# Kernel tuning notes

Measured on AMD Instinct MI355X. Metric: run time of the kernel, lower is better.

The kernel has to match this reference:

```python
import jax, jax.numpy as jnp
import numpy as np

NEG_INF = -9e15


def setup_inputs() -> dict:
    key = jax.random.key(0)
    k1, k2, k3, k4 = jax.random.split(key, 4)
    N, F_in, H, F_out = 4096, 512, 8, 64
    node_features = jax.random.normal(k1, (N, F_in), dtype=jnp.float32)
    adj_matrix = jax.random.randint(k2, (N, N), 0, 2, dtype=jnp.int32)
    # ensure self-loops so every row has at least one unmasked entry
    adj_matrix = jnp.maximum(adj_matrix, jnp.eye(N, dtype=jnp.int32))
    W = jax.random.normal(k3, (H, F_in, F_out), dtype=jnp.float32) * 0.05
    a = jax.random.normal(k4, (H, 2 * F_out), dtype=jnp.float32) * 0.05
    return {"node_features": node_features, "adj_matrix": adj_matrix, "W": W, "a": a}


def reference(node_features, adj_matrix, W, a):
    alpha = 0.2
    H, F_in, F_out = W.shape
    # Per-head linear projection: [H, N, F_out]
    Wh = jnp.einsum("nf,hfo->hno", node_features, W)
    # Attention logits e_ij = LeakyReLU(a1 . Wh_i + a2 . Wh_j)
    f_src = jnp.einsum("hno,ho->hn", Wh, a[:, :F_out])   # [H, N]
    f_dst = jnp.einsum("hno,ho->hn", Wh, a[:, F_out:])   # [H, N]
    e = jax.nn.leaky_relu(f_src[:, :, None] + f_dst[:, None, :], negative_slope=alpha)  # [H, N, N]
    # Mask by adjacency, softmax over neighbors
    masked = jnp.where(adj_matrix[None, :, :] > 0, e, NEG_INF)
    attn = jax.nn.softmax(masked, axis=-1)               # [H, N, N]
    # Aggregate neighbor features per head
    h_prime = jnp.einsum("hnm,hmo->hno", attn, Wh)       # [H, N, F_out]
    # Concat heads along feature dim -> [N, H*F_out]
    return jnp.transpose(h_prime, (1, 0, 2)).reshape(h_prime.shape[1], H * F_out)
```

## Files before the change

kernel.cpp:

```cpp
#include <hip/hip_runtime.h>
#include <stdint.h>


#define NN 4096
#define FIN 512
#define NH 8
#define FO 64

typedef _Float16 f16x8 __attribute__((ext_vector_type(8)));
typedef _Float16 f16x2 __attribute__((ext_vector_type(2)));
typedef __attribute__((ext_vector_type(4))) float f32x4;

union H8 { f16x8 v; f16x2 p[4]; unsigned u[4]; };
union U2 { unsigned u; f16x2 v; };

#define GLOAD_LDS16(g, l)                                                          \
  __builtin_amdgcn_global_load_lds((__attribute__((address_space(1))) const void*)(g), \
                                   (__attribute__((address_space(3))) void*)(l), 16, 0, 0)
#define GLOAD_LDS4(g, l)                                                           \
  __builtin_amdgcn_global_load_lds((__attribute__((address_space(1))) const void*)(g), \
                                   (__attribute__((address_space(3))) void*)(l), 4, 0, 0)

__device__ __forceinline__ unsigned short f2h(float f) {
  _Float16 h = (_Float16)f;
  return __builtin_bit_cast(unsigned short, h);
}

__global__ __launch_bounds__(256) void prep_kernel(
    const float* __restrict__ X, const int* __restrict__ adj, const float* __restrict__ W,
    const float* __restrict__ a,
    unsigned short* __restrict__ Xh, unsigned short* __restrict__ WbT,
    unsigned* __restrict__ adjbitsT, unsigned short* __restrict__ WAh) {
  int bid = blockIdx.x, tid = threadIdx.x;
  if (bid < 2048) {
    int item = bid * 256 + tid;
    int jt = item >> 12, r = item & 4095;
    const int* p = adj + (size_t)r * NN + jt * 32;
    unsigned bits = 0;
#pragma unroll
    for (int b = 0; b < 32; b += 4) {
      int4 v = *(const int4*)(p + b);
      bits |= (unsigned)(v.x & 1) << b;
      bits |= (unsigned)(v.y & 1) << (b + 1);
      bits |= (unsigned)(v.z & 1) << (b + 2);
      bits |= (unsigned)(v.w & 1) << (b + 3);
    }
    adjbitsT[item] = bits;
  } else if (bid < 4096) {
    int item = (bid - 2048) * 256 + tid;
    float4 v = ((const float4*)X)[item];
    ushort4 o;
    o.x = f2h(v.x); o.y = f2h(v.y); o.z = f2h(v.z); o.w = f2h(v.w);
    ((ushort4*)Xh)[item] = o;
  } else if (bid < 5120) {
    int item = (bid - 4096) * 256 + tid;
    int h = item >> 15, rem = item & 32767, o = rem >> 9, k = rem & 511;
    WbT[item] = f2h(W[h * (FIN * FO) + k * FO + o]);
  } else {
    int item = (bid - 5120) * 256 + tid;
    int h = item >> 10, which = (item >> 9) & 1, k = item & 511;
    const float4* wp = (const float4*)(W + ((size_t)h * FIN + k) * FO);
    const float4* ap = (const float4*)(a + h * 128 + which * 64);
    float s = 0.f;
#pragma unroll
    for (int o4 = 0; o4 < 16; ++o4) {
      float4 w4 = wp[o4], a4 = ap[o4];
      s += w4.x * a4.x + w4.y * a4.y + w4.z * a4.z + w4.w * a4.w;
    }
    WAh[(h * 2 + which) * FIN + k] = f2h(s);
  }
}

__global__ __launch_bounds__(256, 4) void proj_sd_kernel(
    const unsigned short* __restrict__ Xh, const unsigned short* __restrict__ WbT,
    const unsigned short* __restrict__ WAh,
    unsigned short* __restrict__ Whfrag, float2* __restrict__ ABf,
    unsigned short* __restrict__ E1h, unsigned short* __restrict__ E2h) {
  int lane = threadIdx.x & 63, wave = threadIdx.x >> 6;
  int row16 = lane & 15, grp = lane >> 4;
  if (blockIdx.y == 8) {
    int i0 = (blockIdx.x * 4 + wave) * 16;
    f32x4 acc = {0, 0, 0, 0};
    const unsigned short* xb = Xh + (size_t)(i0 + row16) * FIN + grp * 8;
    const unsigned short* wb = WAh + row16 * FIN + grp * 8;
#pragma unroll
    for (int k0 = 0; k0 < FIN; k0 += 32)
      acc = __builtin_amdgcn_mfma_f32_16x16x32_f16(*(const f16x8*)(xb + k0),
                                                   *(const f16x8*)(wb + k0), acc, 0, 0, 0);
    int hh = row16 >> 1;
#pragma unroll
    for (int reg = 0; reg < 4; ++reg) {
      int rr = i0 + grp * 4 + reg;
      float v = acc[reg];
      if (row16 & 1) {
        E1h[hh * NN + rr] = f2h(__expf(v));
        E2h[hh * NN + rr] = f2h(__expf(0.2f * v));
      } else {
        ABf[hh * NN + rr] = make_float2(__expf(v), __expf(0.2f * v));
      }
    }
    return;
  }
  int h = blockIdx.y;
  int i0 = blockIdx.x * 64 + wave * 16;
  f32x4 acc[4] = {{0,0,0,0},{0,0,0,0},{0,0,0,0},{0,0,0,0}};
  const unsigned short* xb = Xh + (size_t)(i0 + row16) * FIN + grp * 8;
  const unsigned short* wb = WbT + h * (FO * FIN) + row16 * FIN + grp * 8;
#pragma unroll 4
  for (int k0 = 0; k0 < FIN; k0 += 32) {
    f16x8 af = *(const f16x8*)(xb + k0);
#pragma unroll
    for (int cb = 0; cb < 4; ++cb)
      acc[cb] = __builtin_amdgcn_mfma_f32_16x16x32_f16(
          af, *(const f16x8*)(wb + cb * 16 * FIN + k0), acc[cb], 0, 0, 0);
  }
  int jt = i0 >> 5;
  int kk0 = (i0 & 31) + grp * 4;
  int tl = (kk0 >> 3) * 16 + row16;
  int e0 = kk0 & 7;
#pragma unroll
  for (int cb = 0; cb < 4; ++cb) {
    ushort4 pk;
    pk.x = f2h(acc[cb][0]); pk.y = f2h(acc[cb][1]);
    pk.z = f2h(acc[cb][2]); pk.w = f2h(acc[cb][3]);
    *(ushort4*)(Whfrag + (((size_t)h * 128 + jt) * 4 + cb) * 512 + tl * 8 + e0) = pk;
  }
}

#define SEGB 4608
#define E_OFF 4096
#define A_OFF 4224

__global__ __launch_bounds__(512, 8) void gat_kernel(
    const unsigned* __restrict__ adjbitsT, const unsigned short* __restrict__ Whfrag,
    const float2* __restrict__ ABf, const unsigned short* __restrict__ E1h,
    const unsigned short* __restrict__ E2h, float* __restrict__ out) {
  __shared__ __align__(16) char lds[8 * SEGB];
  int h = blockIdx.y;
  int lane = threadIdx.x & 63, wave = threadIdx.x >> 6;
  int row16 = lane & 15, grp = lane >> 4;
  int rt = wave >> 2, jseg = wave & 3;
  int r0 = blockIdx.x * 32;
  int i0 = r0 + rt * 16;
  int r = i0 + row16;
  float2 ab = ABf[h * NN + r];
  _Float16 Ah1 = (_Float16)(0.5f * ab.x);
  _Float16 Bh1 = (_Float16)(0.5f * ab.y);
  f16x2 Ah = {Ah1, Ah1}, Bh = {Bh1, Bh1};

  H8 ones;
#pragma unroll
  for (int k = 0; k < 4; ++k) ones.u[k] = 0x3C003C00u;

  const unsigned short* wsrc =
      Whfrag + (size_t)h * 262144 + (size_t)jseg * 32 * 2048 + lane * 8;
  const unsigned short* esrc =
      ((lane & 4) ? E2h : E1h) + h * NN + jseg * 1024 + (lane & 3) * 8;
  const unsigned* asrc = adjbitsT + (size_t)(jseg * 32) * NN + r0 + lane;

  f32x4 a0 = {0,0,0,0}, a1 = {0,0,0,0}, a2 = {0,0,0,0}, ad = {0,0,0,0}, aden = {0,0,0,0};

  char* seg0 = lds + (jseg * 2 + 0) * SEGB;
  char* seg1 = lds + (jseg * 2 + 1) * SEGB;

  auto stage = [&](char* seg, int p) {
    if (rt == 0) {
      const unsigned short* bs = wsrc + (size_t)p * 2048;
      GLOAD_LDS16(bs, seg);
      GLOAD_LDS16(bs + 512, seg + 1024);
      GLOAD_LDS16(bs + 1024, seg + 2048);
      GLOAD_LDS16(bs + 1536, seg + 3072);
    } else {
      if (lane < 32) GLOAD_LDS4(asrc + (size_t)p * NN, seg + A_OFF);
      if (lane < 8)  GLOAD_LDS16(esrc + p * 32, seg + E_OFF);
    }
  };

  auto compute = [&](const char* seg) {
    unsigned bw = *(const unsigned*)(seg + A_OFF + (rt * 16 + row16) * 4);
    unsigned bb = (bw >> (grp * 8)) & 0xffu;
    unsigned t32 = bb | (bb << 15);
    H8 e1, e2;
    e1.v = *(const f16x8*)(seg + E_OFF + grp * 16);
    e2.v = *(const f16x8*)(seg + E_OFF + 64 + grp * 16);
    const char* bp = seg + lane * 16;
    f16x8 b0 = *(const f16x8*)(bp);
    f16x8 b1 = *(const f16x8*)(bp + 1024);
    f16x8 b2 = *(const f16x8*)(bp + 2048);
    f16x8 b3 = *(const f16x8*)(bp + 3072);
    H8 af;
#pragma unroll
    for (int k = 0; k < 4; ++k) {
      U2 m;
      m.u = (t32 << (14 - 2 * k)) & 0x40004000u;
      af.p[k] = __builtin_elementwise_max(Ah * e1.p[k], Bh * e2.p[k]) * m.v;
    }
    a0   = __builtin_amdgcn_mfma_f32_16x16x32_f16(af.v, b0, a0, 0, 0, 0);
    a1   = __builtin_amdgcn_mfma_f32_16x16x32_f16(af.v, b1, a1, 0, 0, 0);
    a2   = __builtin_amdgcn_mfma_f32_16x16x32_f16(af.v, b2, a2, 0, 0, 0);
    aden = __builtin_amdgcn_mfma_f32_16x16x32_f16(af.v, ones.v, aden, 0, 0, 0);
    ad   = __builtin_amdgcn_mfma_f32_16x16x32_f16(af.v, b3, ad, 0, 0, 0);
  };

  stage(seg0, 0);
  __syncthreads();
#pragma unroll 1
  for (int p2 = 0; p2 < 16; ++p2) {
    stage(seg1, 2 * p2 + 1);
    compute(seg0);
    __syncthreads();
    if (p2 < 15) stage(seg0, 2 * p2 + 2);
    compute(seg1);
    __syncthreads();
  }

  float* red = (float*)lds;
  if (jseg != 0) {
    float* q = red + (((jseg - 1) * 2 + rt) * 64 + lane) * 20;
    *(f32x4*)(q +  0) = a0;
    *(f32x4*)(q +  4) = a1;
    *(f32x4*)(q +  8) = a2;
    *(f32x4*)(q + 12) = ad;
    *(f32x4*)(q + 16) = aden;
  }
  __syncthreads();
  if (jseg == 0) {
#pragma unroll
    for (int s = 0; s < 3; ++s) {
      const float* q = red + ((s * 2 + rt) * 64 + lane) * 20;
      a0   += *(const f32x4*)(q +  0);
      a1   += *(const f32x4*)(q +  4);
      a2   += *(const f32x4*)(q +  8);
      ad   += *(const f32x4*)(q + 12);
      aden += *(const f32x4*)(q + 16);
    }
#pragma unroll
    for (int reg = 0; reg < 4; ++reg) {
      float inv = 1.0f / aden[reg];
      int row = i0 + grp * 4 + reg;
      float* op = out + (size_t)row * (NH * FO) + h * FO + row16;
      op[0]  = a0[reg] * inv;
      op[16] = a1[reg] * inv;
      op[32] = a2[reg] * inv;
      op[48] = ad[reg] * inv;
    }
  }
}

extern "C" void kernel_launch(void* const* d_in, const int* in_sizes, int n_in,
                              void* d_out, int out_size, void* d_ws, size_t ws_size,
                              hipStream_t stream) {
  const float* X  = (const float*)d_in[0];
  const int* adj  = (const int*)d_in[1];
  const float* W  = (const float*)d_in[2];
  const float* a  = (const float*)d_in[3];
  float* out = (float*)d_out;
  char* ws = (char*)d_ws;

  unsigned short* Xh     = (unsigned short*)(ws + 0);
  unsigned short* WbT    = (unsigned short*)(ws + 4194304);
  unsigned* adjbitsT     = (unsigned*)(ws + 4718592);
  unsigned short* Whfrag = (unsigned short*)(ws + 6815744);
  unsigned short* WAh    = (unsigned short*)(ws + 11010048);
  float2* ABf            = (float2*)(ws + 11026432);
  unsigned short* E1h    = (unsigned short*)(ws + 11288576);
  unsigned short* E2h    = (unsigned short*)(ws + 11354112);

  prep_kernel<<<5152, 256, 0, stream>>>(X, adj, W, a, Xh, WbT, adjbitsT, WAh);
  proj_sd_kernel<<<dim3(64, 9), 256, 0, stream>>>(Xh, WbT, WAh, Whfrag, ABf, E1h, E2h);
  gat_kernel<<<dim3(128, 8), 512, 0, stream>>>(adjbitsT, Whfrag, ABf, E1h, E2h, out);
}
```

Measured before the change: 84.69 us.

## Split-K projection waves and process both row tiles per wave in GAT

The projection kernel now splits the K dimension across two wave groups, reduces the partial sums through LDS, and runs on a flat grid with 512-thread blocks. The attention kernel drops to 4 waves per block, and each wave computes both 16-row tiles. This reuses each loaded B fragment and attention coefficient across twice the rows and cuts LDS reads per MFMA. In exchange, register pressure rises from doubled accumulators and there are fewer waves for latency hiding.

```diff
diff --git a/kernel.cpp b/kernel.cpp
--- a/kernel.cpp
+++ b/kernel.cpp
@@ -71,15 +71,17 @@
   }
 }
 
-__global__ __launch_bounds__(256, 4) void proj_sd_kernel(
+__global__ __launch_bounds__(512, 4) void proj_sd_kernel(
     const unsigned short* __restrict__ Xh, const unsigned short* __restrict__ WbT,
     const unsigned short* __restrict__ WAh,
     unsigned short* __restrict__ Whfrag, float2* __restrict__ ABf,
     unsigned short* __restrict__ E1h, unsigned short* __restrict__ E2h) {
+  __shared__ float red[4 * 64 * 20];
   int lane = threadIdx.x & 63, wave = threadIdx.x >> 6;
   int row16 = lane & 15, grp = lane >> 4;
-  if (blockIdx.y == 8) {
-    int i0 = (blockIdx.x * 4 + wave) * 16;
+  int bx = blockIdx.x;
+  if (bx >= 512) {
+    int i0 = ((bx - 512) * 8 + wave) * 16;
     f32x4 acc = {0, 0, 0, 0};
     const unsigned short* xb = Xh + (size_t)(i0 + row16) * FIN + grp * 8;
     const unsigned short* wb = WAh + row16 * FIN + grp * 8;
@@ -101,29 +103,42 @@
     }
     return;
   }
-  int h = blockIdx.y;
-  int i0 = blockIdx.x * 64 + wave * 16;
+  int kh = wave >> 2, jb = wave & 3;
+  int job = bx * 4 + jb;
+  int h = job & 7, rt = job >> 3;
+  int i0 = rt * 16;
   f32x4 acc[4] = {{0,0,0,0},{0,0,0,0},{0,0,0,0},{0,0,0,0}};
-  const unsigned short* xb = Xh + (size_t)(i0 + row16) * FIN + grp * 8;
-  const unsigned short* wb = WbT + h * (FO * FIN) + row16 * FIN + grp * 8;
-#pragma unroll 4
-  for (int k0 = 0; k0 < FIN; k0 += 32) {
+  const unsigned short* xb = Xh + (size_t)(i0 + row16) * FIN + kh * 256 + grp * 8;
+  const unsigned short* wb = WbT + h * (FO * FIN) + row16 * FIN + kh * 256 + grp * 8;
+#pragma unroll
+  for (int k0 = 0; k0 < 256; k0 += 32) {
     f16x8 af = *(const f16x8*)(xb + k0);
 #pragma unroll
     for (int cb = 0; cb < 4; ++cb)
       acc[cb] = __builtin_amdgcn_mfma_f32_16x16x32_f16(
           af, *(const f16x8*)(wb + cb * 16 * FIN + k0), acc[cb], 0, 0, 0);
   }
-  int jt = i0 >> 5;
-  int kk0 = (i0 & 31) + grp * 4;
-  int tl = (kk0 >> 3) * 16 + row16;
-  int e0 = kk0 & 7;
-#pragma unroll
-  for (int cb = 0; cb < 4; ++cb) {
-    ushort4 pk;
-    pk.x = f2h(acc[cb][0]); pk.y = f2h(acc[cb][1]);
-    pk.z = f2h(acc[cb][2]); pk.w = f2h(acc[cb][3]);
-    *(ushort4*)(Whfrag + (((size_t)h * 128 + jt) * 4 + cb) * 512 + tl * 8 + e0) = pk;
+  if (kh == 1) {
+    float* q = red + (jb * 64 + lane) * 20;
+#pragma unroll
+    for (int cb = 0; cb < 4; ++cb) *(f32x4*)(q + cb * 4) = acc[cb];
+  }
+  __syncthreads();
+  if (kh == 0) {
+    const float* q = red + (jb * 64 + lane) * 20;
+#pragma unroll
+    for (int cb = 0; cb < 4; ++cb) acc[cb] += *(const f32x4*)(q + cb * 4);
+    int jt = i0 >> 5;
+    int kk0 = (i0 & 31) + grp * 4;
+    int tl = (kk0 >> 3) * 16 + row16;
+    int e0 = kk0 & 7;
+#pragma unroll
+    for (int cb = 0; cb < 4; ++cb) {
+      ushort4 pk;
+      pk.x = f2h(acc[cb][0]); pk.y = f2h(acc[cb][1]);
+      pk.z = f2h(acc[cb][2]); pk.w = f2h(acc[cb][3]);
+      *(ushort4*)(Whfrag + (((size_t)h * 128 + jt) * 4 + cb) * 512 + tl * 8 + e0) = pk;
+    }
   }
 }
 
@@ -131,22 +146,20 @@
 #define E_OFF 4096
 #define A_OFF 4224
 
-__global__ __launch_bounds__(512, 8) void gat_kernel(
+__global__ __launch_bounds__(256, 4) void gat_kernel(
     const unsigned* __restrict__ adjbitsT, const unsigned short* __restrict__ Whfrag,
     const float2* __restrict__ ABf, const unsigned short* __restrict__ E1h,
     const unsigned short* __restrict__ E2h, float* __restrict__ out) {
   __shared__ __align__(16) char lds[8 * SEGB];
   int h = blockIdx.y;
-  int lane = threadIdx.x & 63, wave = threadIdx.x >> 6;
+  int lane = threadIdx.x & 63, jseg = threadIdx.x >> 6;
   int row16 = lane & 15, grp = lane >> 4;
-  int rt = wave >> 2, jseg = wave & 3;
   int r0 = blockIdx.x * 32;
-  int i0 = r0 + rt * 16;
-  int r = i0 + row16;
-  float2 ab = ABf[h * NN + r];
-  _Float16 Ah1 = (_Float16)(0.5f * ab.x);
-  _Float16 Bh1 = (_Float16)(0.5f * ab.y);
-  f16x2 Ah = {Ah1, Ah1}, Bh = {Bh1, Bh1};
+  float2 abL = ABf[h * NN + r0 + row16];
+  float2 abH = ABf[h * NN + r0 + 16 + row16];
+  _Float16 aL = (_Float16)(0.5f * abL.x), bL = (_Float16)(0.5f * abL.y);
+  _Float16 aH = (_Float16)(0.5f * abH.x), bH = (_Float16)(0.5f * abH.y);
+  f16x2 AhL = {aL, aL}, BhL = {bL, bL}, AhH = {aH, aH}, BhH = {bH, bH};
 
   H8 ones;
 #pragma unroll
@@ -158,28 +171,29 @@
       ((lane & 4) ? E2h : E1h) + h * NN + jseg * 1024 + (lane & 3) * 8;
   const unsigned* asrc = adjbitsT + (size_t)(jseg * 32) * NN + r0 + lane;
 
-  f32x4 a0 = {0,0,0,0}, a1 = {0,0,0,0}, a2 = {0,0,0,0}, ad = {0,0,0,0}, aden = {0,0,0,0};
+  f32x4 l0 = {0,0,0,0}, l1 = {0,0,0,0}, l2 = {0,0,0,0}, ld = {0,0,0,0}, lden = {0,0,0,0};
+  f32x4 h0 = {0,0,0,0}, h1 = {0,0,0,0}, h2 = {0,0,0,0}, hd = {0,0,0,0}, hden = {0,0,0,0};
 
   char* seg0 = lds + (jseg * 2 + 0) * SEGB;
   char* seg1 = lds + (jseg * 2 + 1) * SEGB;
 
   auto stage = [&](char* seg, int p) {
-    if (rt == 0) {
-      const unsigned short* bs = wsrc + (size_t)p * 2048;
-      GLOAD_LDS16(bs, seg);
-      GLOAD_LDS16(bs + 512, seg + 1024);
-      GLOAD_LDS16(bs + 1024, seg + 2048);
-      GLOAD_LDS16(bs + 1536, seg + 3072);
-    } else {
-      if (lane < 32) GLOAD_LDS4(asrc + (size_t)p * NN, seg + A_OFF);
-      if (lane < 8)  GLOAD_LDS16(esrc + p * 32, seg + E_OFF);
-    }
+    const unsigned short* bs = wsrc + (size_t)p * 2048;
+    GLOAD_LDS16(bs, seg);
+    GLOAD_LDS16(bs + 512, seg + 1024);
+    GLOAD_LDS16(bs + 1024, seg + 2048);
+    GLOAD_LDS16(bs + 1536, seg + 3072);
+    if (lane < 32) GLOAD_LDS4(asrc + (size_t)p * NN, seg + A_OFF);
+    if (lane < 8)  GLOAD_LDS16(esrc + p * 32, seg + E_OFF);
   };
 
   auto compute = [&](const char* seg) {
-    unsigned bw = *(const unsigned*)(seg + A_OFF + (rt * 16 + row16) * 4);
-    unsigned bb = (bw >> (grp * 8)) & 0xffu;
-    unsigned t32 = bb | (bb << 15);
+    unsigned bwL = *(const unsigned*)(seg + A_OFF + row16 * 4);
+    unsigned bwH = *(const unsigned*)(seg + A_OFF + 64 + row16 * 4);
+    unsigned bbL = (bwL >> (grp * 8)) & 0xffu;
+    unsigned bbH = (bwH >> (grp * 8)) & 0xffu;
+    unsigned tL = bbL | (bbL << 15);
+    unsigned tH = bbH | (bbH << 15);
     H8 e1, e2;
     e1.v = *(const f16x8*)(seg + E_OFF + grp * 16);
     e2.v = *(const f16x8*)(seg + E_OFF + 64 + grp * 16);
@@ -188,18 +202,27 @@
     f16x8 b1 = *(const f16x8*)(bp + 1024);
     f16x8 b2 = *(const f16x8*)(bp + 2048);
     f16x8 b3 = *(const f16x8*)(bp + 3072);
-    H8 af;
+    H8 afL, afH;
 #pragma unroll
     for (int k = 0; k < 4; ++k) {
-      U2 m;
-      m.u = (t32 << (14 - 2 * k)) & 0x40004000u;
-      af.p[k] = __builtin_elementwise_max(Ah * e1.p[k], Bh * e2.p[k]) * m.v;
-    }
-    a0   = __builtin_amdgcn_mfma_f32_16x16x32_f16(af.v, b0, a0, 0, 0, 0);
-    a1   = __builtin_amdgcn_mfma_f32_16x16x32_f16(af.v, b1, a1, 0, 0, 0);
-    a2   = __builtin_amdgcn_mfma_f32_16x16x32_f16(af.v, b2, a2, 0, 0, 0);
-    aden = __builtin_amdgcn_mfma_f32_16x16x32_f16(af.v, ones.v, aden, 0, 0, 0);
-    ad   = __builtin_amdgcn_mfma_f32_16x16x32_f16(af.v, b3, ad, 0, 0, 0);
+      f16x2 mxL = __builtin_elementwise_max(AhL * e1.p[k], BhL * e2.p[k]);
+      f16x2 mxH = __builtin_elementwise_max(AhH * e1.p[k], BhH * e2.p[k]);
+      U2 mL, mH;
+      mL.u = (tL << (14 - 2 * k)) & 0x40004000u;
+      mH.u = (tH << (14 - 2 * k)) & 0x40004000u;
+      afL.p[k] = mxL * mL.v;
+      afH.p[k] = mxH * mH.v;
+    }
+    l0   = __builtin_amdgcn_mfma_f32_16x16x32_f16(afL.v, b0, l0, 0, 0, 0);
+    l1   = __builtin_amdgcn_mfma_f32_16x16x32_f16(afL.v, b1, l1, 0, 0, 0);
+    l2   = __builtin_amdgcn_mfma_f32_16x16x32_f16(afL.v, b2, l2, 0, 0, 0);
+    ld   = __builtin_amdgcn_mfma_f32_16x16x32_f16(afL.v, b3, ld, 0, 0, 0);
+    lden = __builtin_amdgcn_mfma_f32_16x16x32_f16(afL.v, ones.v, lden, 0, 0, 0);
+    h0   = __builtin_amdgcn_mfma_f32_16x16x32_f16(afH.v, b0, h0, 0, 0, 0);
+    h1   = __builtin_amdgcn_mfma_f32_16x16x32_f16(afH.v, b1, h1, 0, 0, 0);
+    h2   = __builtin_amdgcn_mfma_f32_16x16x32_f16(afH.v, b2, h2, 0, 0, 0);
+    hd   = __builtin_amdgcn_mfma_f32_16x16x32_f16(afH.v, b3, hd, 0, 0, 0);
+    hden = __builtin_amdgcn_mfma_f32_16x16x32_f16(afH.v, ones.v, hden, 0, 0, 0);
   };
 
   stage(seg0, 0);
@@ -216,33 +239,38 @@
 
   float* red = (float*)lds;
   if (jseg != 0) {
-    float* q = red + (((jseg - 1) * 2 + rt) * 64 + lane) * 20;
-    *(f32x4*)(q +  0) = a0;
-    *(f32x4*)(q +  4) = a1;
-    *(f32x4*)(q +  8) = a2;
-    *(f32x4*)(q + 12) = ad;
-    *(f32x4*)(q + 16) = aden;
+    float* q = red + ((jseg - 1) * 64 + lane) * 40;
+    *(f32x4*)(q +  0) = l0;  *(f32x4*)(q +  4) = l1;
+    *(f32x4*)(q +  8) = l2;  *(f32x4*)(q + 12) = ld;
+    *(f32x4*)(q + 16) = lden;
+    *(f32x4*)(q + 20) = h0;  *(f32x4*)(q + 24) = h1;
+    *(f32x4*)(q + 28) = h2;  *(f32x4*)(q + 32) = hd;
+    *(f32x4*)(q + 36) = hden;
   }
   __syncthreads();
   if (jseg == 0) {
 #pragma unroll
     for (int s = 0; s < 3; ++s) {
-      const float* q = red + ((s * 2 + rt) * 64 + lane) * 20;
-      a0   += *(const f32x4*)(q +  0);
-      a1   += *(const f32x4*)(q +  4);
-      a2   += *(const f32x4*)(q +  8);
-      ad   += *(const f32x4*)(q + 12);
-      aden += *(const f32x4*)(q + 16);
+      const float* q = red + (s * 64 + lane) * 40;
+      l0   += *(const f32x4*)(q +  0);  l1   += *(const f32x4*)(q +  4);
+      l2   += *(const f32x4*)(q +  8);  ld   += *(const f32x4*)(q + 12);
+      lden += *(const f32x4*)(q + 16);
+      h0   += *(const f32x4*)(q + 20);  h1   += *(const f32x4*)(q + 24);
+      h2   += *(const f32x4*)(q + 28);  hd   += *(const f32x4*)(q + 32);
+      hden += *(const f32x4*)(q + 36);
     }
 #pragma unroll
     for (int reg = 0; reg < 4; ++reg) {
-      float inv = 1.0f / aden[reg];
-      int row = i0 + grp * 4 + reg;
-      float* op = out + (size_t)row * (NH * FO) + h * FO + row16;
-      op[0]  = a0[reg] * inv;
-      op[16] = a1[reg] * inv;
-      op[32] = a2[reg] * inv;
-      op[48] = ad[reg] * inv;
+      float invL = 1.0f / lden[reg];
+      float invH = 1.0f / hden[reg];
+      int rowL = r0 + grp * 4 + reg;
+      int rowH = r0 + 16 + grp * 4 + reg;
+      float* opL = out + (size_t)rowL * (NH * FO) + h * FO + row16;
+      float* opH = out + (size_t)rowH * (NH * FO) + h * FO + row16;
+      opL[0]  = l0[reg] * invL;  opL[16] = l1[reg] * invL;
+      opL[32] = l2[reg] * invL;  opL[48] = ld[reg] * invL;
+      opH[0]  = h0[reg] * invH;  opH[16] = h1[reg] * invH;
+      opH[32] = h2[reg] * invH;  opH[48] = hd[reg] * invH;
     }
   }
 }
@@ -267,6 +295,6 @@
   unsigned short* E2h    = (unsigned short*)(ws + 11354112);
 
   prep_kernel<<<5152, 256, 0, stream>>>(X, adj, W, a, Xh, WbT, adjbitsT, WAh);
-  proj_sd_kernel<<<dim3(64, 9), 256, 0, stream>>>(Xh, WbT, WAh, Whfrag, ABf, E1h, E2h);
-  gat_kernel<<<dim3(128, 8), 512, 0, stream>>>(adjbitsT, Whfrag, ABf, E1h, E2h, out);
-}
+  proj_sd_kernel<<<544, 512, 0, stream>>>(Xh, WbT, WAh, Whfrag, ABf, E1h, E2h);
+  gat_kernel<<<dim3(128, 8), 256, 0, stream>>>(adjbitsT, Whfrag, ABf, E1h, E2h, out);
+}
```

After: 85.57 us. No clear change (+1.0%).
